# Performance work log

Hardware: AMD Instinct MI355X
Metric: run time of the kernel (lower is better)

The kernel has to match this reference:

```python
import jax, jax.numpy as jnp
import numpy as np

HIDDEN = 2048
NUM_HEADS = 16
HEAD_DIM = 128
INNER = NUM_HEADS * HEAD_DIM
ROPE_BASE = 10000.0


def apply_rope(x):
    # x: [B, H, S, D], rotate-half (NeoX-style) RoPE
    B, H, S, D = x.shape
    inv_freq = 1.0 / (ROPE_BASE ** (jnp.arange(0, D, 2, dtype=jnp.float32) / D))
    t = jnp.arange(S, dtype=jnp.float32)
    freqs = t[:, None] * inv_freq[None, :]          # [S, D/2]
    cos = jnp.concatenate([jnp.cos(freqs)] * 2, -1)  # [S, D]
    sin = jnp.concatenate([jnp.sin(freqs)] * 2, -1)
    x1, x2 = x[..., : D // 2], x[..., D // 2:]
    rotated = jnp.concatenate([-x2, x1], axis=-1)
    return x * cos[None, None] + rotated * sin[None, None]


def setup_inputs() -> dict:
    key = jax.random.key(0)
    ks = jax.random.split(key, 9)
    s = 1.0 / np.sqrt(HIDDEN)
    return {
        "hidden_states": jax.random.normal(ks[0], (2, 2048, HIDDEN), jnp.float32),
        "Wq": jax.random.uniform(ks[1], (INNER, HIDDEN), jnp.float32, -s, s),
        "bq": jax.random.uniform(ks[2], (INNER,), jnp.float32, -s, s),
        "Wk": jax.random.uniform(ks[3], (INNER, HIDDEN), jnp.float32, -s, s),
        "bk": jax.random.uniform(ks[4], (INNER,), jnp.float32, -s, s),
        "Wv": jax.random.uniform(ks[5], (INNER, HIDDEN), jnp.float32, -s, s),
        "bv": jax.random.uniform(ks[6], (INNER,), jnp.float32, -s, s),
        "Wo": jax.random.uniform(ks[7], (HIDDEN, INNER), jnp.float32, -s, s),
        "bo": jax.random.uniform(ks[8], (HIDDEN,), jnp.float32, -s, s),
    }


def reference(hidden_states, Wq, bq, Wk, bk, Wv, bv, Wo, bo):
    B, S, _ = hidden_states.shape

    def heads(x):  # [B,S,inner] -> [B,H,S,D]
        return x.reshape(B, S, NUM_HEADS, HEAD_DIM).transpose(0, 2, 1, 3)

    q = heads(hidden_states @ Wq.T + bq)
    k = heads(hidden_states @ Wk.T + bk)
    v = heads(hidden_states @ Wv.T + bv)
    q = apply_rope(q)
    k = apply_rope(k)

    scores = jnp.einsum("bhqd,bhkd->bhqk", q, k) / jnp.sqrt(
        jnp.asarray(HEAD_DIM, q.dtype))
    causal = jnp.tril(jnp.ones((S, S), dtype=bool))
    scores = jnp.where(causal[None, None], scores, jnp.finfo(scores.dtype).min)
    weights = jax.nn.softmax(scores, axis=-1)
    context = jnp.einsum("bhqk,bhkd->bhqd", weights, v)
    merged = context.transpose(0, 2, 1, 3).reshape(B, S, INNER)
    return merged @ Wo.T + bo
```

## Files before the change

kernel.cpp:

```cpp
#include <hip/hip_runtime.h>

using u16 = unsigned short;
using u32 = unsigned int;

typedef __attribute__((ext_vector_type(4))) float f32x4;
typedef __attribute__((ext_vector_type(8))) short frag8;

#define HIDDEN 2048
#define SEQ    2048
#define NHEADS 16
#define HDIM   128

__device__ __forceinline__ float bf2f(u16 u) {
  union { u32 i; float f; } c; c.i = ((u32)u) << 16; return c.f;
}
__device__ __forceinline__ u16 f2bf(float f) {
  union { float f; u32 i; } c; c.f = f;
  u32 u = c.i + 0x7fffu + ((c.i >> 16) & 1u);
  return (u16)(u >> 16);
}

__global__ void cvt_all(const float* __restrict__ X,
                        const float* __restrict__ W0, const float* __restrict__ W1,
                        const float* __restrict__ W2, const float* __restrict__ W3,
                        u16* __restrict__ dX,
                        u16* __restrict__ dW0, u16* __restrict__ dW1,
                        u16* __restrict__ dW2, u16* __restrict__ dW3)
{
  const int bx = blockIdx.x;
  const float* s; u16* d; int g;
  if (bx < 4096) { s = X; d = dX; g = bx * 256 + threadIdx.x; }
  else {
    const int t = bx - 4096;
    const int w = t >> 11;
    s = (w == 0) ? W0 : (w == 1) ? W1 : (w == 2) ? W2 : W3;
    d = (w == 0) ? dW0 : (w == 1) ? dW1 : (w == 2) ? dW2 : dW3;
    g = (t & 2047) * 256 + threadIdx.x;
  }
  const float* p = s + (size_t)g * 8;
  f32x4 x0 = *(const f32x4*)p, x1 = *(const f32x4*)(p + 4);
  frag8 o;
#pragma unroll
  for (int e = 0; e < 4; e++) { o[e] = (short)f2bf(x0[e]); o[e+4] = (short)f2bf(x1[e]); }
  *(frag8*)(d + (size_t)g * 8) = o;
}

template<int W_BF16, int NW, int VT, int C_F32>
__global__ __launch_bounds__(256, 4)
void gemm_fused(const u16* __restrict__ A,
                const void* __restrict__ W0, const void* __restrict__ W1,
                const void* __restrict__ W2,
                const float* __restrict__ bias0, const float* __restrict__ bias1,
                const float* __restrict__ bias2,
                void* __restrict__ C0, void* __restrict__ C1, void* __restrict__ C2)
{
  __shared__ __align__(16) u16 smem[8192];
  u16* As = smem;
  u16* Bs = smem + 4096;

  const int tid  = threadIdx.x;
  const int lane = tid & 63;
  const int wv   = tid >> 6;
  const int quad = lane >> 4;
  const int l16  = lane & 15;
  const int wm = wv >> 1, wn = wv & 1;
  const int m0 = blockIdx.y * 128;
  const int wix = (NW == 1) ? 0 : (blockIdx.x >> 4);
  const int n0  = ((NW == 1) ? blockIdx.x : (blockIdx.x & 15)) * 128;

  const void* Wp = (wix == 0) ? W0 : (wix == 1) ? W1 : W2;
  const float* bias = (wix == 0) ? bias0 : (wix == 1) ? bias1 : bias2;
  void* Cp = (wix == 0) ? C0 : (wix == 1) ? C1 : C2;

  f32x4 acc[4][4];
#pragma unroll
  for (int i = 0; i < 4; i++)
#pragma unroll
    for (int j = 0; j < 4; j++) acc[i][j] = (f32x4)0.0f;

  const int g0 = tid, g1 = tid + 256;
  const int r0 = g0 >> 2, c0 = (g0 & 3) * 8;
  const int r1 = g1 >> 2, c1 = (g1 & 3) * 8;

  for (int k0 = 0; k0 < HIDDEN; k0 += 32) {
    __builtin_amdgcn_global_load_lds(
      (const __attribute__((address_space(1))) void*)(A + (size_t)(m0 + r0) * HIDDEN + k0 + c0),
      (__attribute__((address_space(3))) void*)(As + g0 * 8), 16, 0, 0);
    __builtin_amdgcn_global_load_lds(
      (const __attribute__((address_space(1))) void*)(A + (size_t)(m0 + r1) * HIDDEN + k0 + c1),
      (__attribute__((address_space(3))) void*)(As + g1 * 8), 16, 0, 0);
    if (W_BF16) {
      const u16* Wb = (const u16*)Wp;
      __builtin_amdgcn_global_load_lds(
        (const __attribute__((address_space(1))) void*)(Wb + (size_t)(n0 + r0) * HIDDEN + k0 + c0),
        (__attribute__((address_space(3))) void*)(Bs + g0 * 8), 16, 0, 0);
      __builtin_amdgcn_global_load_lds(
        (const __attribute__((address_space(1))) void*)(Wb + (size_t)(n0 + r1) * HIDDEN + k0 + c1),
        (__attribute__((address_space(3))) void*)(Bs + g1 * 8), 16, 0, 0);
    } else {
      const float* Wf = (const float*)Wp;
      const float* p0 = Wf + (size_t)(n0 + r0) * HIDDEN + k0 + c0;
      const float* p1 = Wf + (size_t)(n0 + r1) * HIDDEN + k0 + c1;
      f32x4 x0 = *(const f32x4*)p0, x1 = *(const f32x4*)(p0 + 4);
      f32x4 y0 = *(const f32x4*)p1, y1 = *(const f32x4*)(p1 + 4);
      frag8 b0v, b1v;
#pragma unroll
      for (int e = 0; e < 4; e++) {
        b0v[e]   = (short)f2bf(x0[e]); b0v[e+4] = (short)f2bf(x1[e]);
        b1v[e]   = (short)f2bf(y0[e]); b1v[e+4] = (short)f2bf(y1[e]);
      }
      *(frag8*)&Bs[g0 * 8] = b0v;
      *(frag8*)&Bs[g1 * 8] = b1v;
    }

    __builtin_amdgcn_s_waitcnt(0);
    __syncthreads();

    frag8 af[4], bfr[4];
#pragma unroll
    for (int mt = 0; mt < 4; mt++)
      af[mt] = *(const frag8*)&As[(wm*64 + mt*16 + l16) * 32 + quad*8];
#pragma unroll
    for (int nt = 0; nt < 4; nt++)
      bfr[nt] = *(const frag8*)&Bs[(wn*64 + nt*16 + l16) * 32 + quad*8];
#pragma unroll
    for (int mt = 0; mt < 4; mt++)
#pragma unroll
      for (int nt = 0; nt < 4; nt++)
        acc[mt][nt] = __builtin_amdgcn_mfma_f32_16x16x32_bf16(af[mt], bfr[nt], acc[mt][nt], 0, 0, 0);

    __syncthreads();
  }

  if (VT && wix == 2) {
    u16* Cv = (u16*)Cp;
    u16* T = smem + wv * 1056;
#pragma unroll
    for (int nt = 0; nt < 4; nt++) {
      const int n  = n0 + wn*64 + nt*16 + l16;
      const float bv = bias[n];
#pragma unroll
      for (int mt = 0; mt < 4; mt++)
#pragma unroll
        for (int r = 0; r < 4; r++)
          T[l16 * 66 + mt*16 + quad*4 + r] = f2bf(acc[mt][nt][r] + bv);
#pragma unroll
      for (int rr = 0; rr < 16; rr++) {
        const int nn = n0 + wn*64 + nt*16 + rr;
        const int mm = m0 + wm*64 + lane;
        const int b = mm >> 11, s = mm & 2047;
        Cv[((size_t)(b * HIDDEN + nn)) * SEQ + s] = T[rr * 66 + lane];
      }
    }
  } else {
#pragma unroll
    for (int nt = 0; nt < 4; nt++) {
      const int n  = n0 + wn*64 + nt*16 + l16;
      const float bv = bias[n];
#pragma unroll
      for (int mt = 0; mt < 4; mt++) {
#pragma unroll
        for (int r = 0; r < 4; r++) {
          const int m = m0 + wm*64 + mt*16 + quad*4 + r;
          if (C_F32) ((float*)Cp)[(size_t)m * HIDDEN + n] = acc[mt][nt][r] + bv;
          else       ((u16*)Cp)[(size_t)m * HIDDEN + n]   = f2bf(acc[mt][nt][r] + bv);
        }
      }
    }
  }
}

__global__ void rope_kernel(u16* __restrict__ Q, u16* __restrict__ K)
{
  const int tid = blockIdx.x * 256 + threadIdx.x;
  const int t   = tid >> 19;
  const int r   = tid & 524287;
  const int row = r >> 7;
  const int grp = r & 127;
  const int h   = grp >> 3, d0 = (grp & 7) * 8;
  u16* X = t ? K : Q;
  const float s = (float)(row & 2047);
  const float qscale = t ? 1.0f : 0.08838834764831845f;
  const size_t base = (size_t)row * HIDDEN + h * HDIM + d0;
  frag8 a = *(const frag8*)(X + base);
  frag8 b = *(const frag8*)(X + base + 64);
  frag8 oa, ob;
#pragma unroll
  for (int e = 0; e < 8; e++) {
    const float inv = __expf(-(float)(d0 + e) * (9.210340371976184f / 64.0f));
    float sn, c;
    __sincosf(s * inv, &sn, &c);
    const float x1 = bf2f((u16)a[e]), x2 = bf2f((u16)b[e]);
    oa[e] = (short)f2bf((x1 * c - x2 * sn) * qscale);
    ob[e] = (short)f2bf((x2 * c + x1 * sn) * qscale);
  }
  *(frag8*)(X + base)      = oa;
  *(frag8*)(X + base + 64) = ob;
}

#define KS_STR 132
#define VS_STR 68
#define PS_STR 68
__global__ __launch_bounds__(256, 3)
void attn_kernel(const u16* Q, const u16* __restrict__ K,
                 const u16* __restrict__ Vt, u16* O)
{
  __shared__ __align__(16) u16 Ks[64 * KS_STR];
  __shared__ __align__(16) u16 Vs[128 * VS_STR];
  __shared__ __align__(16) u16 Ps[4 * 16 * PS_STR];

  const int bx = blockIdx.x;
  const int g  = bx >> 5;
  const int bh = bx & 31;
  const int qt = (g & 1) ? (31 - (g >> 1)) : (g >> 1);
  const int b = bh >> 4, h = bh & 15;

  const int tid = threadIdx.x, lane = tid & 63, wv = tid >> 6;
  const int quad = lane >> 4, l16 = lane & 15;

  frag8 qf[4];
  const size_t qbase = ((size_t)(b * SEQ) + qt*64 + wv*16) * HIDDEN + h * HDIM;
#pragma unroll
  for (int ks = 0; ks < 4; ks++)
    qf[ks] = *(const frag8*)(Q + qbase + (size_t)l16 * HIDDEN + ks*32 + quad*8);

  f32x4 Oacc[8];
#pragma unroll
  for (int dt = 0; dt < 8; dt++) Oacc[dt] = (f32x4)0.0f;
  float m_i[4], l_i[4];
#pragma unroll
  for (int r = 0; r < 4; r++) { m_i[r] = -1e30f; l_i[r] = 0.0f; }

  const int ktmax = qt + 1;
  const size_t krow0 = (size_t)(b * SEQ) * HIDDEN + h * HDIM;
  const size_t vrow0 = (size_t)(b * HIDDEN + h * HDIM) * SEQ;
  u16* Pw = Ps + wv * (16 * PS_STR);
  const int qmin = qt*64 + wv*16;

  for (int kt = 0; kt < ktmax; kt++) {
#pragma unroll
    for (int it = 0; it < 4; it++) {
      const int G = it * 256 + tid;
      const int key = G >> 4, gd = (G & 15) * 8;
      *(frag8*)&Ks[key * KS_STR + gd] =
        *(const frag8*)(K + krow0 + (size_t)(kt*64 + key) * HIDDEN + gd);
    }
#pragma unroll
    for (int it = 0; it < 4; it++) {
      const int G = it * 256 + tid;
      const int d = G >> 3, j8 = (G & 7) * 8;
      *(frag8*)&Vs[d * VS_STR + j8] =
        *(const frag8*)(Vt + vrow0 + (size_t)d * SEQ + kt*64 + j8);
    }
    __syncthreads();

    f32x4 st[4];
#pragma unroll
    for (int jt = 0; jt < 4; jt++) st[jt] = (f32x4)0.0f;

#pragma unroll
    for (int ks = 0; ks < 4; ks++) {
      frag8 kf[4];
#pragma unroll
      for (int jt = 0; jt < 4; jt++)
        kf[jt] = *(const frag8*)&Ks[(jt*16 + l16) * KS_STR + ks*32 + quad*8];
#pragma unroll
      for (int jt = 0; jt < 4; jt++)
        st[jt] = __builtin_amdgcn_mfma_f32_16x16x32_bf16(qf[ks], kf[jt], st[jt], 0, 0, 0);
    }

    if (kt == qt) {
#pragma unroll
      for (int jt = 0; jt < 4; jt++) {
        const int jl = jt*16 + l16;
#pragma unroll
        for (int r = 0; r < 4; r++) {
          const int ml = wv*16 + quad*4 + r;
          st[jt][r] = (jl <= ml) ? st[jt][r] : -1e30f;
        }
      }
    }

    float alpha[4];
#pragma unroll
    for (int r = 0; r < 4; r++) {
      float cm = st[0][r];
#pragma unroll
      for (int jt = 1; jt < 4; jt++) cm = fmaxf(cm, st[jt][r]);
      cm = fmaxf(cm, __shfl_xor(cm, 1, 64));
      cm = fmaxf(cm, __shfl_xor(cm, 2, 64));
      cm = fmaxf(cm, __shfl_xor(cm, 4, 64));
      cm = fmaxf(cm, __shfl_xor(cm, 8, 64));
      const float mnew = fmaxf(m_i[r], cm);
      alpha[r] = __expf(m_i[r] - mnew);
      m_i[r] = mnew;
    }

    float csum[4];
#pragma unroll
    for (int r = 0; r < 4; r++) csum[r] = 0.0f;
#pragma unroll
    for (int jt = 0; jt < 4; jt++)
#pragma unroll
      for (int r = 0; r < 4; r++) {
        const float p = __expf(st[jt][r] - m_i[r]);
        csum[r] += p;
        Pw[(quad*4 + r) * PS_STR + jt*16 + l16] = f2bf(p);
      }
#pragma unroll
    for (int r = 0; r < 4; r++) {
      float cs = csum[r];
      cs += __shfl_xor(cs, 1, 64);
      cs += __shfl_xor(cs, 2, 64);
      cs += __shfl_xor(cs, 4, 64);
      cs += __shfl_xor(cs, 8, 64);
      l_i[r] = l_i[r] * alpha[r] + cs;
#pragma unroll
      for (int dt = 0; dt < 8; dt++) Oacc[dt][r] *= alpha[r];
    }

#pragma unroll
    for (int ks2 = 0; ks2 < 2; ks2++) {
      frag8 pf = *(const frag8*)&Pw[l16 * PS_STR + ks2*32 + quad*8];
#pragma unroll
      for (int dt = 0; dt < 8; dt++) {
        frag8 vf = *(const frag8*)&Vs[(dt*16 + l16) * VS_STR + ks2*32 + quad*8];
        Oacc[dt] = __builtin_amdgcn_mfma_f32_16x16x32_bf16(pf, vf, Oacc[dt], 0, 0, 0);
      }
    }
    __syncthreads();
  }

#pragma unroll
  for (int r = 0; r < 4; r++) {
    const float inv = 1.0f / l_i[r];
    const int m = qmin + quad*4 + r;
#pragma unroll
    for (int dt = 0; dt < 8; dt++) {
      const int d = dt*16 + l16;
      O[((size_t)(b * SEQ) + m) * HIDDEN + h * HDIM + d] = f2bf(Oacc[dt][r] * inv);
    }
  }
}

extern "C" void kernel_launch(void* const* d_in, const int* in_sizes, int n_in,
                              void* d_out, int out_size, void* d_ws, size_t ws_size,
                              hipStream_t stream)
{
  const float* X  = (const float*)d_in[0];
  const float* Wq = (const float*)d_in[1];
  const float* bq = (const float*)d_in[2];
  const float* Wk = (const float*)d_in[3];
  const float* bk = (const float*)d_in[4];
  const float* Wv = (const float*)d_in[5];
  const float* bv = (const float*)d_in[6];
  const float* Wo = (const float*)d_in[7];
  const float* bo = (const float*)d_in[8];
  float* out = (float*)d_out;

  u16* Kb = (u16*)d_out;
  u16* Xb = (u16*)d_out + (8u << 20);
  char* ws = (char*)d_ws;
  u16* Qb  = (u16*)ws;
  u16* Vtb = (u16*)(ws + (16u << 20));

  dim3 blk(256);
  const bool fast = ws_size >= (64u << 20);
  if (fast) {
    u16* Wqb = (u16*)(ws + (32u << 20));
    u16* Wkb = (u16*)(ws + (40u << 20));
    u16* Wvb = (u16*)(ws + (48u << 20));
    u16* Wob = (u16*)(ws + (56u << 20));
    cvt_all<<<12288, blk, 0, stream>>>(X, Wq, Wk, Wv, Wo, Xb, Wqb, Wkb, Wvb, Wob);
    gemm_fused<1,3,1,0><<<dim3(48,32), blk, 0, stream>>>(
        Xb, Wqb, Wkb, Wvb, bq, bk, bv, Qb, Kb, Vtb);
    rope_kernel<<<4096, blk, 0, stream>>>(Qb, Kb);
    attn_kernel<<<1024, blk, 0, stream>>>(Qb, Kb, Vtb, Qb);
    gemm_fused<1,1,0,1><<<dim3(16,32), blk, 0, stream>>>(
        Qb, Wob, Wob, Wob, bo, bo, bo, out, out, out);
  } else {
    cvt_all<<<4096, blk, 0, stream>>>(X, Wq, Wk, Wv, Wo, Xb, Xb, Xb, Xb, Xb);
    gemm_fused<0,3,1,0><<<dim3(48,32), blk, 0, stream>>>(
        Xb, Wq, Wk, Wv, bq, bk, bv, Qb, Kb, Vtb);
    rope_kernel<<<4096, blk, 0, stream>>>(Qb, Kb);
    attn_kernel<<<1024, blk, 0, stream>>>(Qb, Kb, Vtb, Qb);
    gemm_fused<0,1,0,1><<<dim3(16,32), blk, 0, stream>>>(
        Qb, Wo, Wo, Wo, bo, bo, bo, out, out, out);
  }
}
```

Measured before the change: 439.7 us.

## Replace QKV GEMM with 256x128-tile, 512-thread triple-buffered LDS-DMA kernel

Adds a dedicated QKV projection GEMM that uses 256x128 output tiles with 8 waves. It triple-buffers K-slices in LDS, filled by direct global-to-LDS loads with an XOR swizzle, and interleaves barriers and s_setprio around the MFMA bursts. Blocks are remapped so neighbouring blocks share weight tiles. The aim is more reuse per tile, latency hidden behind compute, and fewer register staging copies. In exchange it uses about 144KB of LDS per block, carries heavy register pressure, and its hand-tuned waitcnt logic is fragile.

Measured after the change: 428.3 us. 1.03x faster.

```diff
diff --git a/kernel.cpp b/kernel.cpp
--- a/kernel.cpp
+++ b/kernel.cpp
@@ -170,6 +170,151 @@
   }
 }
 
+#define NT32 32
+
+#define STG(gptr, lofs) __builtin_amdgcn_global_load_lds( \
+    (const __attribute__((address_space(1))) void*)(gptr), \
+    (__attribute__((address_space(3))) void*)(smem + (lofs)), 16, 0, 0)
+
+#define GRP(t, DOSTAGE, WAITSTR) { \
+  u16* As = smem + ((t) % 3) * 24576; \
+  u16* Bs = As + 16384; \
+  frag8 af[8], bfr[2]; \
+  _Pragma("unroll") for (int mt = 0; mt < 8; mt++) \
+    af[mt] = *(const frag8*)(As + abase + mt*1024 + s0q); \
+  bfr[0] = *(const frag8*)(Bs + bbase + s0q); \
+  bfr[1] = *(const frag8*)(Bs + bbase + 1024 + s0q); \
+  if (DOSTAGE) { \
+    const size_t ko = (size_t)((t)+2)*64; const int sb = (((t)+2)%3)*24576; \
+    STG(gA0 + ko, sb + ldsA0); STG(gA1 + ko, sb + ldsA1); STG(gB0 + ko, sb + ldsB0); \
+  } \
+  __builtin_amdgcn_s_barrier(); \
+  __builtin_amdgcn_s_setprio(1); \
+  _Pragma("unroll") for (int mt = 0; mt < 8; mt++) { \
+    acc[mt][0] = __builtin_amdgcn_mfma_f32_16x16x32_bf16(af[mt], bfr[0], acc[mt][0], 0,0,0); \
+    acc[mt][1] = __builtin_amdgcn_mfma_f32_16x16x32_bf16(af[mt], bfr[1], acc[mt][1], 0,0,0); \
+  } \
+  __builtin_amdgcn_s_setprio(0); \
+  __builtin_amdgcn_s_barrier(); \
+  _Pragma("unroll") for (int mt = 0; mt < 8; mt++) \
+    af[mt] = *(const frag8*)(As + abase + mt*1024 + s1q); \
+  bfr[0] = *(const frag8*)(Bs + bbase + s1q); \
+  bfr[1] = *(const frag8*)(Bs + bbase + 1024 + s1q); \
+  if (DOSTAGE) { \
+    const size_t ko = (size_t)((t)+2)*64; const int sb = (((t)+2)%3)*24576; \
+    STG(gA2 + ko, sb + ldsA2); STG(gA3 + ko, sb + ldsA3); STG(gB1 + ko, sb + ldsB1); \
+  } \
+  __builtin_amdgcn_s_barrier(); \
+  __builtin_amdgcn_s_setprio(1); \
+  _Pragma("unroll") for (int mt = 0; mt < 8; mt++) { \
+    acc[mt][0] = __builtin_amdgcn_mfma_f32_16x16x32_bf16(af[mt], bfr[0], acc[mt][0], 0,0,0); \
+    acc[mt][1] = __builtin_amdgcn_mfma_f32_16x16x32_bf16(af[mt], bfr[1], acc[mt][1], 0,0,0); \
+  } \
+  __builtin_amdgcn_s_setprio(0); \
+  asm volatile("s_waitcnt " WAITSTR ::: "memory"); \
+  __builtin_amdgcn_s_barrier(); \
+}
+
+__global__ __launch_bounds__(512, 2)
+void gemm256_qkv(const u16* __restrict__ A,
+                 const u16* __restrict__ W0, const u16* __restrict__ W1,
+                 const u16* __restrict__ W2,
+                 const float* __restrict__ bias0, const float* __restrict__ bias1,
+                 const float* __restrict__ bias2,
+                 u16* __restrict__ C0, u16* __restrict__ C1, u16* __restrict__ Vt)
+{
+  __shared__ __align__(16) u16 smem[73728];
+
+  const int tid  = threadIdx.x;
+  const int lane = tid & 63;
+  const int wv   = tid >> 6;
+  const int quad = lane >> 4;
+  const int l16  = lane & 15;
+  const int wm = wv >> 2, wn = wv & 3;
+
+  const int bid = blockIdx.x;
+  const int sbid = (bid & 7) * 96 + (bid >> 3);
+  const int colTile = sbid >> 4;
+  const int rowTile = sbid & 15;
+  const int wix = colTile >> 4;
+  const int n0  = (colTile & 15) * 128;
+  const int m0  = rowTile * 256;
+
+  const u16* Wp = (wix == 0) ? W0 : (wix == 1) ? W1 : W2;
+  const float* bias = (wix == 0) ? bias0 : (wix == 1) ? bias1 : bias2;
+
+  const int c8 = (lane & 7) ^ (lane >> 3);
+  const int rA = lane >> 3;
+  const u16* gA0 = A  + (size_t)(m0 + wv*32 +  0 + rA) * HIDDEN + c8*8;
+  const u16* gA1 = A  + (size_t)(m0 + wv*32 +  8 + rA) * HIDDEN + c8*8;
+  const u16* gA2 = A  + (size_t)(m0 + wv*32 + 16 + rA) * HIDDEN + c8*8;
+  const u16* gA3 = A  + (size_t)(m0 + wv*32 + 24 + rA) * HIDDEN + c8*8;
+  const u16* gB0 = Wp + (size_t)(n0 + wv*16 +  0 + rA) * HIDDEN + c8*8;
+  const u16* gB1 = Wp + (size_t)(n0 + wv*16 +  8 + rA) * HIDDEN + c8*8;
+  const int ldsA0 = (4*wv)*512 + lane*8;
+  const int ldsA1 = ldsA0 + 512;
+  const int ldsA2 = ldsA0 + 1024;
+  const int ldsA3 = ldsA0 + 1536;
+  const int ldsB0 = 16384 + (2*wv)*512 + lane*8;
+  const int ldsB1 = ldsB0 + 512;
+
+  const int s0q = ((quad    ) ^ (l16 & 7)) * 8;
+  const int s1q = ((quad + 4) ^ (l16 & 7)) * 8;
+  const int abase = (wm*128 + l16) * 64;
+  const int bbase = (wn*32  + l16) * 64;
+
+  f32x4 acc[8][2];
+#pragma unroll
+  for (int i = 0; i < 8; i++) { acc[i][0] = (f32x4)0.0f; acc[i][1] = (f32x4)0.0f; }
+
+  STG(gA0, ldsA0); STG(gA1, ldsA1); STG(gB0, ldsB0);
+  STG(gA2, ldsA2); STG(gA3, ldsA3); STG(gB1, ldsB1);
+  STG(gA0 + 64, 24576 + ldsA0); STG(gA1 + 64, 24576 + ldsA1); STG(gB0 + 64, 24576 + ldsB0);
+  STG(gA2 + 64, 24576 + ldsA2); STG(gA3 + 64, 24576 + ldsA3); STG(gB1 + 64, 24576 + ldsB1);
+  asm volatile("s_waitcnt vmcnt(6)" ::: "memory");
+  __builtin_amdgcn_s_barrier();
+
+  for (int t = 0; t < NT32 - 2; ++t) GRP(t, 1, "vmcnt(6)");
+  GRP(NT32 - 2, 0, "vmcnt(0)");
+  GRP(NT32 - 1, 0, "vmcnt(63)");
+
+  if (wix != 2) {
+    u16* Cb = (wix == 0) ? C0 : C1;
+#pragma unroll
+    for (int nt = 0; nt < 2; nt++) {
+      const int n = n0 + wn*32 + nt*16 + l16;
+      const float bv = bias[n];
+#pragma unroll
+      for (int mt = 0; mt < 8; mt++) {
+        const int m = m0 + wm*128 + mt*16 + quad*4;
+#pragma unroll
+        for (int r = 0; r < 4; r++)
+          Cb[(size_t)(m + r) * HIDDEN + n] = f2bf(acc[mt][nt][r] + bv);
+      }
+    }
+  } else {
+    u16* T = smem + wv * 2176;
+    const int b  = m0 >> 11;
+    const int s0 = (m0 & 2047) + wm*128;
+#pragma unroll
+    for (int nt = 0; nt < 2; nt++) {
+      const int nloc = n0 + wn*32 + nt*16;
+      const float bv = bias[nloc + l16];
+#pragma unroll
+      for (int mt = 0; mt < 8; mt++)
+#pragma unroll
+        for (int r = 0; r < 4; r++)
+          T[l16*136 + mt*16 + quad*4 + r] = f2bf(acc[mt][nt][r] + bv);
+#pragma unroll
+      for (int rr = 0; rr < 16; rr++) {
+        const size_t vb = ((size_t)(b * HIDDEN + nloc + rr)) * SEQ + s0;
+        Vt[vb + lane]      = T[rr*136 + lane];
+        Vt[vb + 64 + lane] = T[rr*136 + 64 + lane];
+      }
+    }
+  }
+}
+
 __global__ void rope_kernel(u16* __restrict__ Q, u16* __restrict__ K)
 {
   const int tid = blockIdx.x * 256 + threadIdx.x;
@@ -372,7 +517,7 @@
     u16* Wvb = (u16*)(ws + (48u << 20));
     u16* Wob = (u16*)(ws + (56u << 20));
     cvt_all<<<12288, blk, 0, stream>>>(X, Wq, Wk, Wv, Wo, Xb, Wqb, Wkb, Wvb, Wob);
-    gemm_fused<1,3,1,0><<<dim3(48,32), blk, 0, stream>>>(
+    gemm256_qkv<<<dim3(768), dim3(512), 0, stream>>>(
         Xb, Wqb, Wkb, Wvb, bq, bk, bv, Qb, Kb, Vtb);
     rope_kernel<<<4096, blk, 0, stream>>>(Qb, Kb);
     attn_kernel<<<1024, blk, 0, stream>>>(Qb, Kb, Vtb, Qb);
```
